# Kernel tuning notes

Measured on AMD Instinct MI355X. Metric: run time of the kernel, lower is better.

Reference implementation:

```python
import jax, jax.numpy as jnp
import numpy as np

HEADS = 8
DIM_HEAD = 64
SCALE = DIM_HEAD ** -0.5


def setup_inputs() -> dict:
    key = jax.random.key(0)
    ks = jax.random.split(key, 7)
    b, n, m = 2, 4096, 4096
    query_dim, context_dim, inner = 1024, 768, HEADS * DIM_HEAD
    s = 0.02
    return {
        "x": jax.random.normal(ks[0], (b, n, query_dim), jnp.float32),
        "context": jax.random.normal(ks[1], (b, m, context_dim), jnp.float32),
        "Wq": jax.random.normal(ks[2], (query_dim, inner), jnp.float32) * s,
        "Wk": jax.random.normal(ks[3], (context_dim, inner), jnp.float32) * s,
        "Wv": jax.random.normal(ks[4], (context_dim, inner), jnp.float32) * s,
        "Wo": jax.random.normal(ks[5], (inner, query_dim), jnp.float32) * s,
        "bo": jnp.zeros((query_dim,), jnp.float32),
    }


def reference(x, context, Wq, Wk, Wv, Wo, bo):
    b, n, _ = x.shape
    m = context.shape[1]
    # projections (no bias), split heads: b n (h d) -> b n h d
    q = (x @ Wq).reshape(b, n, HEADS, DIM_HEAD)
    k = (context @ Wk).reshape(b, m, HEADS, DIM_HEAD)
    v = (context @ Wv).reshape(b, m, HEADS, DIM_HEAD)
    # fp32 QK^T (ATTN_PRECISION='fp32' path), full [b,h,n,m] scores
    sim = jnp.einsum("bihd,bjhd->bhij", q.astype(jnp.float32), k.astype(jnp.float32)) * SCALE
    attn = jax.nn.softmax(sim, axis=-1).astype(v.dtype)
    out = jnp.einsum("bhij,bjhd->bihd", attn, v).reshape(b, n, HEADS * DIM_HEAD)
    # to_out: Linear with bias (dropout=0 is identity)
    return out @ Wo + bo
```

## Files before the change

### kernel.cpp

```cpp
#include <hip/hip_runtime.h>
#include <hip/hip_bf16.h>
#include <cmath>


using bf16_t = __hip_bfloat16;
typedef __bf16 bf16x8 __attribute__((ext_vector_type(8)));
typedef float  f32x4  __attribute__((ext_vector_type(4)));

static constexpr int BATCH = 2;
static constexpr int NQ    = 4096;
static constexpr int NKV   = 4096;
static constexpr int NH    = 8;
static constexpr int DH    = 64;
static constexpr int INNER = NH * DH;
static constexpr int QDIM  = 1024;
static constexpr int CDIM  = 768;
static constexpr float QSCALE = 0.125f * 1.4426950408889634f;

#define MFMA_BF16(a, b, c) __builtin_amdgcn_mfma_f32_16x16x32_bf16((a), (b), (c), 0, 0, 0)

__device__ __forceinline__ float fast_exp2(float x) {
  return __builtin_amdgcn_exp2f(x);
}

__device__ __forceinline__ void gload16(const bf16_t* g, bf16_t* l) {
  __builtin_amdgcn_global_load_lds((__attribute__((address_space(1))) void*)(g),
                                   (__attribute__((address_space(3))) void*)(l),
                                   16, 0, 0);
}

__global__ __launch_bounds__(256) void cast2_kernel(const float* __restrict__ x,
                                                    bf16_t* __restrict__ xb, int xn8,
                                                    const float* __restrict__ c,
                                                    bf16_t* __restrict__ cb, int cn8) {
  int id = blockIdx.x * 256 + threadIdx.x;
  const float* in;
  bf16_t* out;
  if (id < xn8) {
    in = x; out = xb;
  } else {
    id -= xn8;
    if (id >= cn8) return;
    in = c; out = cb;
  }
  float4 a = ((const float4*)in)[2 * id];
  float4 b = ((const float4*)in)[2 * id + 1];
  bf16_t t[8] = {__float2bfloat16(a.x), __float2bfloat16(a.y), __float2bfloat16(a.z),
                 __float2bfloat16(a.w), __float2bfloat16(b.x), __float2bfloat16(b.y),
                 __float2bfloat16(b.z), __float2bfloat16(b.w)};
  ((uint4*)out)[id] = *(const uint4*)t;
}

__global__ __launch_bounds__(256) void wtrans4_kernel(const float* __restrict__ Wq,
                                                      const float* __restrict__ Wk,
                                                      const float* __restrict__ Wv,
                                                      const float* __restrict__ Wo,
                                                      bf16_t* __restrict__ WqT,
                                                      bf16_t* __restrict__ WkvT,
                                                      bf16_t* __restrict__ WoT) {
  __shared__ float tile[32][33];
  const float* W;
  bf16_t* WT;
  int K, N;
  switch (blockIdx.z) {
    case 0: W = Wq; WT = WqT; K = QDIM; N = INNER; break;
    case 1: W = Wk; WT = WkvT; K = CDIM; N = INNER; break;
    case 2: W = Wv; WT = WkvT + (size_t)INNER * CDIM; K = CDIM; N = INNER; break;
    default: W = Wo; WT = WoT; K = INNER; N = QDIM; break;
  }
  const int bn = blockIdx.x * 32, bk = blockIdx.y * 32;
  if (bn >= N || bk >= K) return;
  const int tx = threadIdx.x & 31, ty = threadIdx.x >> 5;
  for (int yy = ty; yy < 32; yy += 8)
    tile[yy][tx] = W[(size_t)(bk + yy) * N + bn + tx];
  __syncthreads();
  for (int yy = ty; yy < 32; yy += 8)
    WT[(size_t)(bn + yy) * K + bk + tx] = __float2bfloat16(tile[tx][yy]);
}

__device__ __forceinline__ void gemm128_core(const bf16_t* __restrict__ A,
                                             const bf16_t* __restrict__ WT, int K,
                                             int m0, int n0, int tid,
                                             f32x4 (&acc)[4][4],
                                             bf16_t (*As)[128][32],
                                             bf16_t (*Bs)[128][32]) {
  const int lane = tid & 63, wave = tid >> 6;
  const int lane15 = lane & 15, quad = lane >> 4;
  const int wm = (wave >> 1) * 64, wn = (wave & 1) * 64;
  const int srow = tid >> 2;
  const int scol = ((tid & 3) ^ ((srow >> 1) & 3)) * 8;
  const bf16_t* aptr = A + (size_t)(m0 + srow) * K + scol;
  const bf16_t* bptr = WT + (size_t)(n0 + srow) * K + scol;
  bf16_t* const ab = &As[0][wave * 16][0];
  bf16_t* const bb = &Bs[0][wave * 16][0];
  constexpr int BUF = 128 * 32;

  auto stage = [&](int t) {
    const int c = (t % 3) * BUF;
    const bf16_t* as = aptr + t * 32;
    const bf16_t* bs = bptr + t * 32;
    gload16(as, ab + c);
    gload16(as + (size_t)64 * K, ab + c + 64 * 32);
    gload16(bs, bb + c);
    gload16(bs + (size_t)64 * K, bb + c + 64 * 32);
  };

  const int T = K / 32;
  stage(0);
  stage(1);
  for (int t = 0; t < T; ++t) {
    const int cur = t % 3;
    if (t < T - 1) {
      asm volatile("s_waitcnt vmcnt(4)" ::: "memory");
    } else {
      asm volatile("s_waitcnt vmcnt(0)" ::: "memory");
    }
    asm volatile("s_barrier" ::: "memory");
    if (t + 2 < T) stage(t + 2);
    bf16x8 af[4], bfr[4];
#pragma unroll
    for (int i = 0; i < 4; ++i) {
      const int row = wm + i * 16 + lane15;
      af[i] = *reinterpret_cast<const bf16x8*>(
          &As[cur][0][0] + row * 32 + ((quad * 8) ^ (((row >> 1) & 3) * 8)));
    }
#pragma unroll
    for (int j = 0; j < 4; ++j) {
      const int row = wn + j * 16 + lane15;
      bfr[j] = *reinterpret_cast<const bf16x8*>(
          &Bs[cur][0][0] + row * 32 + ((quad * 8) ^ (((row >> 1) & 3) * 8)));
    }
#pragma unroll
    for (int i = 0; i < 4; ++i)
#pragma unroll
      for (int j = 0; j < 4; ++j) acc[i][j] = MFMA_BF16(af[i], bfr[j], acc[i][j]);
  }
}

__global__ __launch_bounds__(256, 3) void qkv_gemm_kernel(const bf16_t* __restrict__ xb,
                                                          const bf16_t* __restrict__ ctxb,
                                                          const bf16_t* __restrict__ WqT,
                                                          const bf16_t* __restrict__ WkvT,
                                                          bf16_t* __restrict__ qob,
                                                          bf16_t* __restrict__ kb,
                                                          bf16_t* __restrict__ vtb) {
  __shared__ __align__(16) bf16_t As[3][128][32];
  __shared__ __align__(16) bf16_t Bs[3][128][32];
  const int tid = threadIdx.x;
  const bool isq = blockIdx.y < 4;
  const bf16_t* A  = isq ? xb : ctxb;
  const bf16_t* WT = isq ? WqT : WkvT;
  const int K  = isq ? QDIM : CDIM;
  const int m0 = blockIdx.x * 128;
  const int n0 = (isq ? blockIdx.y : blockIdx.y - 4) * 128;

  const f32x4 vzero = {0.f, 0.f, 0.f, 0.f};
  f32x4 acc[4][4];
  for (int i = 0; i < 4; ++i)
    for (int j = 0; j < 4; ++j) acc[i][j] = vzero;

  gemm128_core(A, WT, K, m0, n0, tid, acc, As, Bs);

  const int lane = tid & 63, wave = tid >> 6;
  const int lane15 = lane & 15, quad = lane >> 4;
  const int wm = (wave >> 1) * 64, wn = (wave & 1) * 64;
  for (int i = 0; i < 4; ++i) {
    int gm = m0 + wm + i * 16 + quad * 4;
    for (int j = 0; j < 4; ++j) {
      int gn = n0 + wn + j * 16 + lane15;
      for (int r = 0; r < 4; ++r) {
        float v = acc[i][j][r];
        if (isq) {
          qob[(size_t)(gm + r) * INNER + gn] = __float2bfloat16(v * QSCALE);
        } else if (gn < INNER) {
          kb[(size_t)(gm + r) * INNER + gn] = __float2bfloat16(v);
        } else {
          int gmr = gm + r;
          vtb[((size_t)(gmr >> 12) * INNER + (gn - INNER)) * (size_t)NKV +
              (gmr & 4095)] = __float2bfloat16(v);
        }
      }
    }
  }
}

__global__ __launch_bounds__(256, 3) void out_gemm_kernel(const bf16_t* __restrict__ A,
                                                          const bf16_t* __restrict__ WT,
                                                          float* __restrict__ C,
                                                          const float* __restrict__ bias) {
  __shared__ __align__(16) bf16_t As[3][128][32];
  __shared__ __align__(16) bf16_t Bs[3][128][32];
  const int tid = threadIdx.x;
  const int m0 = blockIdx.x * 128, n0 = blockIdx.y * 128;
  constexpr int K = INNER, N = QDIM;

  const f32x4 vzero = {0.f, 0.f, 0.f, 0.f};
  f32x4 acc[4][4];
  for (int i = 0; i < 4; ++i)
    for (int j = 0; j < 4; ++j) acc[i][j] = vzero;

  gemm128_core(A, WT, K, m0, n0, tid, acc, As, Bs);

  const int lane = tid & 63, wave = tid >> 6;
  const int lane15 = lane & 15, quad = lane >> 4;
  const int wm = (wave >> 1) * 64, wn = (wave & 1) * 64;
  float bv[4];
  for (int j = 0; j < 4; ++j) bv[j] = bias[n0 + wn + j * 16 + lane15];
  for (int i = 0; i < 4; ++i) {
    int gm = m0 + wm + i * 16 + quad * 4;
    for (int j = 0; j < 4; ++j) {
      int gn = n0 + wn + j * 16 + lane15;
      for (int r = 0; r < 4; ++r)
        C[(size_t)(gm + r) * N + gn] = acc[i][j][r] + bv[j];
    }
  }
}

__global__ __launch_bounds__(256, 2) void attn_kernel(const bf16_t* Qg ,
                                                      const bf16_t* __restrict__ Kg ,
                                                      const bf16_t* __restrict__ Vtg ,
                                                      bf16_t* Og ) {
  __shared__ __align__(16) bf16_t KsF[2][8][512];
  __shared__ __align__(16) bf16_t VtF[2][8][512];
  __shared__ __align__(16) bf16_t PsA[128][72];

  const int tid = threadIdx.x;
  const int lane = tid & 63, wave = tid >> 6;
  const int lane15 = lane & 15, quad = lane >> 4;
  const int wrow = wave * 32;
  const int q0 = blockIdx.x * 128;
  const int h = blockIdx.y;
  const int b = blockIdx.z;

  const size_t qbase  = ((size_t)b * NQ + q0) * INNER + h * DH;
  const size_t kbase  = ((size_t)b * NKV) * INNER + h * DH;
  const size_t vtbase = ((size_t)(b * NH + h) * DH) * NKV;

  bf16x8 qf[2][2];
  for (int ks = 0; ks < 2; ++ks)
    for (int qh = 0; qh < 2; ++qh)
      qf[ks][qh] = *reinterpret_cast<const bf16x8*>(
          Qg + qbase + (size_t)(wrow + qh * 16 + lane15) * INNER + ks * 32 + quad * 8);

  bf16x8 ones;
  for (int i = 0; i < 8; ++i) ones[i] = (__bf16)1.0f;

  const f32x4 vzero = {0.f, 0.f, 0.f, 0.f};
  f32x4 acc_o[2][4];
  f32x4 acc_l[2];
  for (int qh = 0; qh < 2; ++qh) {
    acc_l[qh] = vzero;
    for (int j = 0; j < 4; ++j) acc_o[qh][j] = vzero;
  }

  const int c0 = wave * 2, c1 = wave * 2 + 1;
  auto kaddr = [&](int c, int kv0) {
    return Kg + kbase + (size_t)(kv0 + (c & 3) * 16 + lane15) * INNER + (c >> 2) * 32 + quad * 8;
  };
  auto vaddr = [&](int c, int kv0) {
    return Vtg + vtbase + (size_t)((c & 3) * 16 + lane15) * NKV + kv0 + (c >> 2) * 32 + quad * 8;
  };
  uint4 kr0 = *(const uint4*)kaddr(c0, 0), kr1 = *(const uint4*)kaddr(c1, 0);
  uint4 vr0 = *(const uint4*)vaddr(c0, 0), vr1 = *(const uint4*)vaddr(c1, 0);

  constexpr int T = NKV / 64;
  for (int t = 0; t < T; ++t) {
    const int cur = t & 1;
    *(uint4*)&KsF[cur][c0][lane * 8] = kr0;
    *(uint4*)&KsF[cur][c1][lane * 8] = kr1;
    *(uint4*)&VtF[cur][c0][lane * 8] = vr0;
    *(uint4*)&VtF[cur][c1][lane * 8] = vr1;
    __syncthreads();

    if (t + 1 < T) {
      const int kv0n = (t + 1) * 64;
      kr0 = *(const uint4*)kaddr(c0, kv0n);
      kr1 = *(const uint4*)kaddr(c1, kv0n);
      vr0 = *(const uint4*)vaddr(c0, kv0n);
      vr1 = *(const uint4*)vaddr(c1, kv0n);
    }

    f32x4 acc_st[2][4];
#pragma unroll
    for (int qh = 0; qh < 2; ++qh)
      for (int j = 0; j < 4; ++j) acc_st[qh][j] = vzero;
    __builtin_amdgcn_s_setprio(1);
#pragma unroll
    for (int ks = 0; ks < 2; ++ks) {
      bf16x8 kf[4];
#pragma unroll
      for (int j = 0; j < 4; ++j)
        kf[j] = *reinterpret_cast<const bf16x8*>(&KsF[cur][ks * 4 + j][lane * 8]);
#pragma unroll
      for (int qh = 0; qh < 2; ++qh)
#pragma unroll
        for (int j = 0; j < 4; ++j)
          acc_st[qh][j] = MFMA_BF16(kf[j], qf[ks][qh], acc_st[qh][j]);
    }
    __builtin_amdgcn_s_setprio(0);

#pragma unroll
    for (int qh = 0; qh < 2; ++qh)
#pragma unroll
      for (int j = 0; j < 4; ++j) {
        bf16_t t4[4];
        for (int r = 0; r < 4; ++r)
          t4[r] = __float2bfloat16(fast_exp2(acc_st[qh][j][r]));
        *(uint2*)&PsA[wrow + qh * 16 + lane15][j * 16 + quad * 4] = *(const uint2*)t4;
      }
    asm volatile("s_waitcnt lgkmcnt(0)" ::: "memory");

    __builtin_amdgcn_s_setprio(1);
#pragma unroll
    for (int ks = 0; ks < 2; ++ks) {
      bf16x8 vf[4];
#pragma unroll
      for (int j = 0; j < 4; ++j)
        vf[j] = *reinterpret_cast<const bf16x8*>(&VtF[cur][ks * 4 + j][lane * 8]);
#pragma unroll
      for (int qh = 0; qh < 2; ++qh) {
        bf16x8 pf = *reinterpret_cast<const bf16x8*>(
            &PsA[wrow + qh * 16 + lane15][ks * 32 + quad * 8]);
        acc_l[qh] = MFMA_BF16(pf, ones, acc_l[qh]);
#pragma unroll
        for (int j = 0; j < 4; ++j) acc_o[qh][j] = MFMA_BF16(pf, vf[j], acc_o[qh][j]);
      }
    }
    __builtin_amdgcn_s_setprio(0);
  }

  for (int qh = 0; qh < 2; ++qh)
    for (int r = 0; r < 4; ++r) {
      float invr = 1.f / acc_l[qh][r];
      int row = wrow + qh * 16 + quad * 4 + r;
      for (int j = 0; j < 4; ++j)
        Og[qbase + (size_t)row * INNER + j * 16 + lane15] =
            __float2bfloat16(acc_o[qh][j][r] * invr);
    }
}

extern "C" void kernel_launch(void* const* d_in, const int* in_sizes, int n_in,
                              void* d_out, int out_size, void* d_ws, size_t ws_size,
                              hipStream_t stream) {
  (void)in_sizes; (void)n_in; (void)out_size; (void)ws_size;
  const float* x   = (const float*)d_in[0];
  const float* ctx = (const float*)d_in[1];
  const float* Wq  = (const float*)d_in[2];
  const float* Wk  = (const float*)d_in[3];
  const float* Wv  = (const float*)d_in[4];
  const float* Wo  = (const float*)d_in[5];
  const float* bo  = (const float*)d_in[6];
  float* out = (float*)d_out;

  char* ws = (char*)d_ws;
  size_t off = 0;
  auto take = [&](size_t nelem) { bf16_t* p = (bf16_t*)(ws + off); off += nelem * 2; return p; };
  bf16_t* WqT  = take((size_t)INNER * QDIM);
  bf16_t* WkvT = take((size_t)(2 * INNER) * CDIM);
  bf16_t* WoT  = take((size_t)QDIM * INNER);
  bf16_t* qob  = take((size_t)BATCH * NQ * INNER);
  bf16_t* kb   = take((size_t)BATCH * NKV * INNER);
  bf16_t* vtb  = take((size_t)BATCH * INNER * NKV);

  bf16_t* xb   = (bf16_t*)d_out;
  bf16_t* ctxb = xb + (size_t)BATCH * NQ * QDIM;

  const int M = BATCH * NQ;
  const int xN8 = BATCH * NQ * QDIM / 8, cN8 = BATCH * NKV * CDIM / 8;

  cast2_kernel<<<(xN8 + cN8 + 255) / 256, 256, 0, stream>>>(x, xb, xN8, ctx, ctxb, cN8);
  wtrans4_kernel<<<dim3(32, 32, 4), 256, 0, stream>>>(Wq, Wk, Wv, Wo, WqT, WkvT, WoT);

  qkv_gemm_kernel<<<dim3(M / 128, 12), 256, 0, stream>>>(xb, ctxb, WqT, WkvT, qob, kb, vtb);

  attn_kernel<<<dim3(NQ / 128, NH, BATCH), 256, 0, stream>>>(qob, kb, vtb, qob);

  out_gemm_kernel<<<dim3(M / 128, QDIM / 128), 256, 0, stream>>>(qob, WoT, out, bo);
}
```

Baseline: 240.0 us.

## Use 32x32 MFMA attention with KV split across waves and register P

Rewrites the attention kernel to run 512 threads per block. Each pair of waves shares 32 query rows and splits each 64-key tile, with one wave per 32-key half. Scores use 32x32x16 bf16 MFMAs. The exponentiated probabilities are packed and rearranged in registers with v_permlane32_swap instead of going through an LDS P buffer, so the P store/load and its waitcnt disappear. Partial outputs and row sums from the two KV halves are combined through shared memory at the end, which adds an extra reduction step and register pressure under launch bounds of (512, 4).

After: 248.9 us. 1.04x slower.

```diff
diff --git a/kernel.cpp b/kernel.cpp
--- a/kernel.cpp
+++ b/kernel.cpp
@@ -1,11 +1,13 @@
 #include <hip/hip_runtime.h>
 #include <hip/hip_bf16.h>
 #include <cmath>
+#include <cstdint>
 
 
 using bf16_t = __hip_bfloat16;
 typedef __bf16 bf16x8 __attribute__((ext_vector_type(8)));
 typedef float  f32x4  __attribute__((ext_vector_type(4)));
+typedef float  f32x16 __attribute__((ext_vector_type(16)));
 
 static constexpr int BATCH = 2;
 static constexpr int NQ    = 4096;
@@ -18,6 +20,7 @@
 static constexpr float QSCALE = 0.125f * 1.4426950408889634f;
 
 #define MFMA_BF16(a, b, c) __builtin_amdgcn_mfma_f32_16x16x32_bf16((a), (b), (c), 0, 0, 0)
+#define MFMA32_BF16(a, b, c) __builtin_amdgcn_mfma_f32_32x32x16_bf16((a), (b), (c), 0, 0, 0)
 
 __device__ __forceinline__ float fast_exp2(float x) {
   return __builtin_amdgcn_exp2f(x);
@@ -27,6 +30,24 @@
   __builtin_amdgcn_global_load_lds((__attribute__((address_space(1))) void*)(g),
                                    (__attribute__((address_space(3))) void*)(l),
                                    16, 0, 0);
+}
+
+__device__ __forceinline__ uint32_t pk2(float lo, float hi) {
+  __hip_bfloat16 a = __float2bfloat16(lo), b = __float2bfloat16(hi);
+  union { unsigned short s[2]; uint32_t u; } x;
+  x.s[0] = *(unsigned short*)&a;
+  x.s[1] = *(unsigned short*)&b;
+  return x.u;
+}
+
+__device__ __forceinline__ void pl32swap(uint32_t& a, uint32_t& b) {
+  asm volatile("v_permlane32_swap_b32 %0, %1" : "+v"(a), "+v"(b));
+}
+
+__device__ __forceinline__ bf16x8 frag4(uint32_t w0, uint32_t w1, uint32_t w2, uint32_t w3) {
+  union { uint32_t w[4]; bf16x8 f; } u;
+  u.w[0] = w0; u.w[1] = w1; u.w[2] = w2; u.w[3] = w3;
+  return u.f;
 }
 
 __global__ __launch_bounds__(256) void cast2_kernel(const float* __restrict__ x,
@@ -216,18 +237,21 @@
   }
 }
 
-__global__ __launch_bounds__(256, 2) void attn_kernel(const bf16_t* Qg ,
+__global__ __launch_bounds__(512, 4) void attn_kernel(const bf16_t* Qg ,
                                                       const bf16_t* __restrict__ Kg ,
                                                       const bf16_t* __restrict__ Vtg ,
                                                       bf16_t* Og ) {
-  __shared__ __align__(16) bf16_t KsF[2][8][512];
-  __shared__ __align__(16) bf16_t VtF[2][8][512];
-  __shared__ __align__(16) bf16_t PsA[128][72];
+  __shared__ __align__(16) char smem[33792];
+  auto KsF = (bf16_t(*)[8][512])smem;
+  auto VtF = (bf16_t(*)[8][512])(smem + 16384);
+  float* scrO = (float*)smem;
+  float* scrL = (float*)(smem + 32768);
 
   const int tid = threadIdx.x;
   const int lane = tid & 63, wave = tid >> 6;
-  const int lane15 = lane & 15, quad = lane >> 4;
-  const int wrow = wave * 32;
+  const int lane31 = lane & 31, hi = lane >> 5;
+  const int qg = wave >> 1;
+  const int v  = wave & 1;
   const int q0 = blockIdx.x * 128;
   const int h = blockIdx.y;
   const int b = blockIdx.z;
@@ -236,107 +260,102 @@
   const size_t kbase  = ((size_t)b * NKV) * INNER + h * DH;
   const size_t vtbase = ((size_t)(b * NH + h) * DH) * NKV;
 
-  bf16x8 qf[2][2];
-  for (int ks = 0; ks < 2; ++ks)
-    for (int qh = 0; qh < 2; ++qh)
-      qf[ks][qh] = *reinterpret_cast<const bf16x8*>(
-          Qg + qbase + (size_t)(wrow + qh * 16 + lane15) * INNER + ks * 32 + quad * 8);
+  bf16x8 qf[4];
+#pragma unroll
+  for (int kc = 0; kc < 4; ++kc)
+    qf[kc] = *reinterpret_cast<const bf16x8*>(
+        Qg + qbase + (size_t)(qg * 32 + lane31) * INNER + kc * 16 + hi * 8);
 
   bf16x8 ones;
+#pragma unroll
   for (int i = 0; i < 8; ++i) ones[i] = (__bf16)1.0f;
 
-  const f32x4 vzero = {0.f, 0.f, 0.f, 0.f};
-  f32x4 acc_o[2][4];
-  f32x4 acc_l[2];
-  for (int qh = 0; qh < 2; ++qh) {
-    acc_l[qh] = vzero;
-    for (int j = 0; j < 4; ++j) acc_o[qh][j] = vzero;
-  }
-
-  const int c0 = wave * 2, c1 = wave * 2 + 1;
-  auto kaddr = [&](int c, int kv0) {
-    return Kg + kbase + (size_t)(kv0 + (c & 3) * 16 + lane15) * INNER + (c >> 2) * 32 + quad * 8;
+  f32x16 acc_o[2];
+  f32x16 acc_l;
+  for (int i = 0; i < 16; ++i) { acc_o[0][i] = 0.f; acc_o[1][i] = 0.f; acc_l[i] = 0.f; }
+
+  const int skv = (wave >> 2) * 32, skc = (wave & 3) * 16;
+  const int sdt = ((wave >> 1) & 1) * 32, skb = (wave & 1) * 16;
+  auto kaddr = [&](int kv0) {
+    return Kg + kbase + (size_t)(kv0 + skv + lane31) * INNER + skc + hi * 8;
   };
-  auto vaddr = [&](int c, int kv0) {
-    return Vtg + vtbase + (size_t)((c & 3) * 16 + lane15) * NKV + kv0 + (c >> 2) * 32 + quad * 8;
+  auto vaddr = [&](int kv0) {
+    return Vtg + vtbase + (size_t)(sdt + lane31) * NKV + kv0 + skv + skb + hi * 8;
   };
-  uint4 kr0 = *(const uint4*)kaddr(c0, 0), kr1 = *(const uint4*)kaddr(c1, 0);
-  uint4 vr0 = *(const uint4*)vaddr(c0, 0), vr1 = *(const uint4*)vaddr(c1, 0);
+  uint4 kr = *(const uint4*)kaddr(0);
+  uint4 vr = *(const uint4*)vaddr(0);
 
   constexpr int T = NKV / 64;
   for (int t = 0; t < T; ++t) {
     const int cur = t & 1;
-    *(uint4*)&KsF[cur][c0][lane * 8] = kr0;
-    *(uint4*)&KsF[cur][c1][lane * 8] = kr1;
-    *(uint4*)&VtF[cur][c0][lane * 8] = vr0;
-    *(uint4*)&VtF[cur][c1][lane * 8] = vr1;
+    *(uint4*)&KsF[cur][wave][lane * 8] = kr;
+    *(uint4*)&VtF[cur][wave][lane * 8] = vr;
     __syncthreads();
 
     if (t + 1 < T) {
-      const int kv0n = (t + 1) * 64;
-      kr0 = *(const uint4*)kaddr(c0, kv0n);
-      kr1 = *(const uint4*)kaddr(c1, kv0n);
-      vr0 = *(const uint4*)vaddr(c0, kv0n);
-      vr1 = *(const uint4*)vaddr(c1, kv0n);
-    }
-
-    f32x4 acc_st[2][4];
-#pragma unroll
-    for (int qh = 0; qh < 2; ++qh)
-      for (int j = 0; j < 4; ++j) acc_st[qh][j] = vzero;
+      kr = *(const uint4*)kaddr((t + 1) * 64);
+      vr = *(const uint4*)vaddr((t + 1) * 64);
+    }
+
+    f32x16 st;
+    for (int i = 0; i < 16; ++i) st[i] = 0.f;
     __builtin_amdgcn_s_setprio(1);
 #pragma unroll
-    for (int ks = 0; ks < 2; ++ks) {
-      bf16x8 kf[4];
-#pragma unroll
-      for (int j = 0; j < 4; ++j)
-        kf[j] = *reinterpret_cast<const bf16x8*>(&KsF[cur][ks * 4 + j][lane * 8]);
-#pragma unroll
-      for (int qh = 0; qh < 2; ++qh)
-#pragma unroll
-        for (int j = 0; j < 4; ++j)
-          acc_st[qh][j] = MFMA_BF16(kf[j], qf[ks][qh], acc_st[qh][j]);
+    for (int kc = 0; kc < 4; ++kc) {
+      bf16x8 kf = *reinterpret_cast<const bf16x8*>(&KsF[cur][v * 4 + kc][lane * 8]);
+      st = MFMA32_BF16(kf, qf[kc], st);
     }
     __builtin_amdgcn_s_setprio(0);
 
-#pragma unroll
-    for (int qh = 0; qh < 2; ++qh)
-#pragma unroll
-      for (int j = 0; j < 4; ++j) {
-        bf16_t t4[4];
-        for (int r = 0; r < 4; ++r)
-          t4[r] = __float2bfloat16(fast_exp2(acc_st[qh][j][r]));
-        *(uint2*)&PsA[wrow + qh * 16 + lane15][j * 16 + quad * 4] = *(const uint2*)t4;
+    uint32_t c0 = pk2(fast_exp2(st[0]),  fast_exp2(st[1]));
+    uint32_t c1 = pk2(fast_exp2(st[2]),  fast_exp2(st[3]));
+    uint32_t c2 = pk2(fast_exp2(st[4]),  fast_exp2(st[5]));
+    uint32_t c3 = pk2(fast_exp2(st[6]),  fast_exp2(st[7]));
+    uint32_t c4 = pk2(fast_exp2(st[8]),  fast_exp2(st[9]));
+    uint32_t c5 = pk2(fast_exp2(st[10]), fast_exp2(st[11]));
+    uint32_t c6 = pk2(fast_exp2(st[12]), fast_exp2(st[13]));
+    uint32_t c7 = pk2(fast_exp2(st[14]), fast_exp2(st[15]));
+    pl32swap(c0, c2);
+    pl32swap(c1, c3);
+    pl32swap(c4, c6);
+    pl32swap(c5, c7);
+    bf16x8 pf0 = frag4(c0, c1, c2, c3);
+    bf16x8 pf1 = frag4(c4, c5, c6, c7);
+
+    __builtin_amdgcn_s_setprio(1);
+    acc_l = MFMA32_BF16(pf0, ones, acc_l);
+    acc_l = MFMA32_BF16(pf1, ones, acc_l);
+#pragma unroll
+    for (int dt = 0; dt < 2; ++dt) {
+      bf16x8 vf0 = *reinterpret_cast<const bf16x8*>(&VtF[cur][v * 4 + dt * 2 + 0][lane * 8]);
+      bf16x8 vf1 = *reinterpret_cast<const bf16x8*>(&VtF[cur][v * 4 + dt * 2 + 1][lane * 8]);
+      acc_o[dt] = MFMA32_BF16(pf0, vf0, acc_o[dt]);
+      acc_o[dt] = MFMA32_BF16(pf1, vf1, acc_o[dt]);
+    }
+    __builtin_amdgcn_s_setprio(0);
+  }
+
+  __syncthreads();
+  if (v == 1) {
+#pragma unroll
+    for (int dt = 0; dt < 2; ++dt)
+      for (int r = 0; r < 16; ++r)
+        scrO[((qg * 2 + dt) * 16 + r) * 64 + lane] = acc_o[dt][r];
+    if (lane31 == 0)
+      for (int r = 0; r < 16; ++r) scrL[(qg * 2 + hi) * 16 + r] = acc_l[r];
+  }
+  __syncthreads();
+  if (v == 0) {
+    for (int r = 0; r < 16; ++r) {
+      float lt = acc_l[r] + scrL[(qg * 2 + hi) * 16 + r];
+      float inv = 1.f / lt;
+      int qrow = qg * 32 + (r & 3) + 8 * (r >> 2) + 4 * hi;
+      for (int dt = 0; dt < 2; ++dt) {
+        float o = acc_o[dt][r] + scrO[((qg * 2 + dt) * 16 + r) * 64 + lane];
+        Og[qbase + (size_t)qrow * INNER + dt * 32 + lane31] = __float2bfloat16(o * inv);
       }
-    asm volatile("s_waitcnt lgkmcnt(0)" ::: "memory");
-
-    __builtin_amdgcn_s_setprio(1);
-#pragma unroll
-    for (int ks = 0; ks < 2; ++ks) {
-      bf16x8 vf[4];
-#pragma unroll
-      for (int j = 0; j < 4; ++j)
-        vf[j] = *reinterpret_cast<const bf16x8*>(&VtF[cur][ks * 4 + j][lane * 8]);
-#pragma unroll
-      for (int qh = 0; qh < 2; ++qh) {
-        bf16x8 pf = *reinterpret_cast<const bf16x8*>(
-            &PsA[wrow + qh * 16 + lane15][ks * 32 + quad * 8]);
-        acc_l[qh] = MFMA_BF16(pf, ones, acc_l[qh]);
-#pragma unroll
-        for (int j = 0; j < 4; ++j) acc_o[qh][j] = MFMA_BF16(pf, vf[j], acc_o[qh][j]);
-      }
-    }
-    __builtin_amdgcn_s_setprio(0);
-  }
-
-  for (int qh = 0; qh < 2; ++qh)
-    for (int r = 0; r < 4; ++r) {
-      float invr = 1.f / acc_l[qh][r];
-      int row = wrow + qh * 16 + quad * 4 + r;
-      for (int j = 0; j < 4; ++j)
-        Og[qbase + (size_t)row * INNER + j * 16 + lane15] =
-            __float2bfloat16(acc_o[qh][j][r] * invr);
-    }
+    }
+  }
 }
 
 extern "C" void kernel_launch(void* const* d_in, const int* in_sizes, int n_in,
@@ -373,7 +392,7 @@
 
   qkv_gemm_kernel<<<dim3(M / 128, 12), 256, 0, stream>>>(xb, ctxb, WqT, WkvT, qob, kb, vtb);
 
-  attn_kernel<<<dim3(NQ / 128, NH, BATCH), 256, 0, stream>>>(qob, kb, vtb, qob);
+  attn_kernel<<<dim3(NQ / 128, NH, BATCH), 512, 0, stream>>>(qob, kb, vtb, qob);
 
   out_gemm_kernel<<<dim3(M / 128, QDIM / 128), 256, 0, stream>>>(qob, WoT, out, bo);
 }
```

## Fuse cast and weight-transpose kernels and remap block IDs across XCDs

Applied to the files above, without the earlier changes.

Merges the activation cast and the weight transpose into a single prep kernel with a flat 1D grid, which removes one kernel launch and the blocks that exited early in the old 3D transpose grid. The GEMM and attention kernels switch to 1D grids with a block-ID swizzle ((bid&7)*stride + bid>>3). This puts neighbouring tiles that share A/B or K/V data on the same XCD, so they can reuse the same L2. The risk is scheduling order effects, and the hardcoded block counts tie the code to these exact shapes.

Result: no change. 242.3 us (median of 2 runs) (+1.0%).

```diff
diff --git a/kernel.cpp b/kernel.cpp
--- a/kernel.cpp
+++ b/kernel.cpp
@@ -1,6 +1,7 @@
 #include <hip/hip_runtime.h>
 #include <hip/hip_bf16.h>
 #include <cmath>
+#include <cstdint>
 
 
 using bf16_t = __hip_bfloat16;
@@ -29,47 +30,54 @@
                                    16, 0, 0);
 }
 
-__global__ __launch_bounds__(256) void cast2_kernel(const float* __restrict__ x,
-                                                    bf16_t* __restrict__ xb, int xn8,
-                                                    const float* __restrict__ c,
-                                                    bf16_t* __restrict__ cb, int cn8) {
-  int id = blockIdx.x * 256 + threadIdx.x;
-  const float* in;
-  bf16_t* out;
-  if (id < xn8) {
-    in = x; out = xb;
-  } else {
-    id -= xn8;
-    if (id >= cn8) return;
-    in = c; out = cb;
-  }
-  float4 a = ((const float4*)in)[2 * id];
-  float4 b = ((const float4*)in)[2 * id + 1];
-  bf16_t t[8] = {__float2bfloat16(a.x), __float2bfloat16(a.y), __float2bfloat16(a.z),
-                 __float2bfloat16(a.w), __float2bfloat16(b.x), __float2bfloat16(b.y),
-                 __float2bfloat16(b.z), __float2bfloat16(b.w)};
-  ((uint4*)out)[id] = *(const uint4*)t;
-}
-
-__global__ __launch_bounds__(256) void wtrans4_kernel(const float* __restrict__ Wq,
-                                                      const float* __restrict__ Wk,
-                                                      const float* __restrict__ Wv,
-                                                      const float* __restrict__ Wo,
-                                                      bf16_t* __restrict__ WqT,
-                                                      bf16_t* __restrict__ WkvT,
-                                                      bf16_t* __restrict__ WoT) {
+__global__ __launch_bounds__(256) void prep_kernel(const float* __restrict__ x,
+                                                   const float* __restrict__ ctx,
+                                                   const float* __restrict__ Wq,
+                                                   const float* __restrict__ Wk,
+                                                   const float* __restrict__ Wv,
+                                                   const float* __restrict__ Wo,
+                                                   bf16_t* __restrict__ xb,
+                                                   bf16_t* __restrict__ ctxb,
+                                                   bf16_t* __restrict__ WqT,
+                                                   bf16_t* __restrict__ WkvT,
+                                                   bf16_t* __restrict__ WoT) {
+  constexpr int XN8 = BATCH * NQ * QDIM / 8;
+  constexpr int CN8 = BATCH * NKV * CDIM / 8;
+  constexpr int CAST_BLK = (XN8 + CN8) / 256;
   __shared__ float tile[32][33];
+  const int bid = blockIdx.x;
+  if (bid < CAST_BLK) {
+    int id = bid * 256 + threadIdx.x;
+    const float* in;
+    bf16_t* out;
+    if (id < XN8) {
+      in = x; out = xb;
+    } else {
+      id -= XN8; in = ctx; out = ctxb;
+    }
+    float4 a = ((const float4*)in)[2 * id];
+    float4 b = ((const float4*)in)[2 * id + 1];
+    bf16_t t[8] = {__float2bfloat16(a.x), __float2bfloat16(a.y), __float2bfloat16(a.z),
+                   __float2bfloat16(a.w), __float2bfloat16(b.x), __float2bfloat16(b.y),
+                   __float2bfloat16(b.z), __float2bfloat16(b.w)};
+    ((uint4*)out)[id] = *(const uint4*)t;
+    return;
+  }
+  int wb = bid - CAST_BLK;
   const float* W;
   bf16_t* WT;
   int K, N;
-  switch (blockIdx.z) {
-    case 0: W = Wq; WT = WqT; K = QDIM; N = INNER; break;
-    case 1: W = Wk; WT = WkvT; K = CDIM; N = INNER; break;
-    case 2: W = Wv; WT = WkvT + (size_t)INNER * CDIM; K = CDIM; N = INNER; break;
-    default: W = Wo; WT = WoT; K = INNER; N = QDIM; break;
-  }
-  const int bn = blockIdx.x * 32, bk = blockIdx.y * 32;
-  if (bn >= N || bk >= K) return;
+  if (wb < 512) {
+    W = Wq; WT = WqT; K = QDIM; N = INNER;
+  } else if (wb < 896) {
+    wb -= 512; W = Wk; WT = WkvT; K = CDIM; N = INNER;
+  } else if (wb < 1280) {
+    wb -= 896; W = Wv; WT = WkvT + (size_t)INNER * CDIM; K = CDIM; N = INNER;
+  } else {
+    wb -= 1280; W = Wo; WT = WoT; K = INNER; N = QDIM;
+  }
+  const int bnt = N / 32;
+  const int bn = (wb % bnt) * 32, bk = (wb / bnt) * 32;
   const int tx = threadIdx.x & 31, ty = threadIdx.x >> 5;
   for (int yy = ty; yy < 32; yy += 8)
     tile[yy][tx] = W[(size_t)(bk + yy) * N + bn + tx];
@@ -147,12 +155,15 @@
   __shared__ __align__(16) bf16_t As[3][128][32];
   __shared__ __align__(16) bf16_t Bs[3][128][32];
   const int tid = threadIdx.x;
-  const bool isq = blockIdx.y < 4;
+  const int bid = blockIdx.x;
+  const int vb = (bid & 7) * 96 + (bid >> 3);
+  const int bx = vb / 12, bsel = vb % 12;
+  const bool isq = bsel < 4;
   const bf16_t* A  = isq ? xb : ctxb;
   const bf16_t* WT = isq ? WqT : WkvT;
   const int K  = isq ? QDIM : CDIM;
-  const int m0 = blockIdx.x * 128;
-  const int n0 = (isq ? blockIdx.y : blockIdx.y - 4) * 128;
+  const int m0 = bx * 128;
+  const int n0 = (isq ? bsel : bsel - 4) * 128;
 
   const f32x4 vzero = {0.f, 0.f, 0.f, 0.f};
   f32x4 acc[4][4];
@@ -191,7 +202,9 @@
   __shared__ __align__(16) bf16_t As[3][128][32];
   __shared__ __align__(16) bf16_t Bs[3][128][32];
   const int tid = threadIdx.x;
-  const int m0 = blockIdx.x * 128, n0 = blockIdx.y * 128;
+  const int bid = blockIdx.x;
+  const int vb = (bid & 7) * 64 + (bid >> 3);
+  const int m0 = (vb >> 3) * 128, n0 = (vb & 7) * 128;
   constexpr int K = INNER, N = QDIM;
 
   const f32x4 vzero = {0.f, 0.f, 0.f, 0.f};
@@ -228,9 +241,11 @@
   const int lane = tid & 63, wave = tid >> 6;
   const int lane15 = lane & 15, quad = lane >> 4;
   const int wrow = wave * 32;
-  const int q0 = blockIdx.x * 128;
-  const int h = blockIdx.y;
-  const int b = blockIdx.z;
+  const int bid = blockIdx.x;
+  const int vb = (bid & 7) * 64 + (bid >> 3);
+  const int qt = vb & 31, hb = vb >> 5;
+  const int h = hb & 7, b = hb >> 3;
+  const int q0 = qt * 128;
 
   const size_t qbase  = ((size_t)b * NQ + q0) * INNER + h * DH;
   const size_t kbase  = ((size_t)b * NKV) * INNER + h * DH;
@@ -243,6 +258,7 @@
           Qg + qbase + (size_t)(wrow + qh * 16 + lane15) * INNER + ks * 32 + quad * 8);
 
   bf16x8 ones;
+#pragma unroll
   for (int i = 0; i < 8; ++i) ones[i] = (__bf16)1.0f;
 
   const f32x4 vzero = {0.f, 0.f, 0.f, 0.f};
@@ -365,15 +381,11 @@
   bf16_t* xb   = (bf16_t*)d_out;
   bf16_t* ctxb = xb + (size_t)BATCH * NQ * QDIM;
 
-  const int M = BATCH * NQ;
-  const int xN8 = BATCH * NQ * QDIM / 8, cN8 = BATCH * NKV * CDIM / 8;
-
-  cast2_kernel<<<(xN8 + cN8 + 255) / 256, 256, 0, stream>>>(x, xb, xN8, ctx, ctxb, cN8);
-  wtrans4_kernel<<<dim3(32, 32, 4), 256, 0, stream>>>(Wq, Wk, Wv, Wo, WqT, WkvT, WoT);
-
-  qkv_gemm_kernel<<<dim3(M / 128, 12), 256, 0, stream>>>(xb, ctxb, WqT, WkvT, qob, kb, vtb);
-
-  attn_kernel<<<dim3(NQ / 128, NH, BATCH), 256, 0, stream>>>(qob, kb, vtb, qob);
-
-  out_gemm_kernel<<<dim3(M / 128, QDIM / 128), 256, 0, stream>>>(qob, WoT, out, bo);
-}
+  prep_kernel<<<8960, 256, 0, stream>>>(x, ctx, Wq, Wk, Wv, Wo, xb, ctxb, WqT, WkvT, WoT);
+
+  qkv_gemm_kernel<<<768, 256, 0, stream>>>(xb, ctxb, WqT, WkvT, qob, kb, vtb);
+
+  attn_kernel<<<512, 256, 0, stream>>>(qob, kb, vtb, qob);
+
+  out_gemm_kernel<<<512, 256, 0, stream>>>(qob, WoT, out, bo);
+}
```
